# Kernel optimization log

Hardware: AMD Instinct MI355X
Metric: run time of the kernel (lower is better)

The kernel has to match this reference:

```python
import jax, jax.numpy as jnp
import numpy as np

G, NPG = 256, 128          # graphs per batch, nodes per graph
N = G * NPG                # 32768 total nodes
E = 524288                 # total directed edges; first half 'in', second half 'out'
DIN, D = 128, 256          # input feature dim, hidden dim
R = 200                    # num relations
C = 2                      # num classes
EPS = 1e-5                 # batchnorm eps


def setup_inputs() -> dict:
    key = jax.random.key(0)
    ks = jax.random.split(key, 20)

    def w(k, shape):
        fan_in = shape[-2] if len(shape) >= 2 else shape[-1]
        return jax.random.normal(k, shape, jnp.float32) / np.float32(np.sqrt(fan_in))

    return {
        "x": jax.random.normal(ks[0], (N, DIN), jnp.float32),
        "rel_emb": w(ks[1], (R, DIN)),
        # conv1: DIN -> D
        "w_in1": w(ks[2], (DIN, D)), "w_out1": w(ks[3], (DIN, D)),
        "w_loop1": w(ks[4], (DIN, D)), "w_rel1": w(ks[5], (DIN, D)),
        "loop_rel1": w(ks[6], (1, DIN)),
        "bias1": jnp.zeros((D,), jnp.float32),
        "gamma1": jnp.ones((D,), jnp.float32), "beta1": jnp.zeros((D,), jnp.float32),
        # conv2..conv5 stacked: D -> D
        "W_in": w(ks[7], (4, D, D)), "W_out": w(ks[8], (4, D, D)),
        "W_loop": w(ks[9], (4, D, D)), "W_rel": w(ks[10], (4, D, D)),
        "Loop_rel": w(ks[11], (4, 1, D)),
        "Bias": jnp.zeros((4, D), jnp.float32),
        "Gamma": jnp.ones((4, D), jnp.float32), "Beta": jnp.zeros((4, D), jnp.float32),
        # head: concat2 => Linear(4*D, C)
        "lin_w": w(ks[12], (4 * D, C)), "lin_b": jnp.zeros((C,), jnp.float32),
        # graph data (int constants)
        "edge_index": jax.random.randint(ks[13], (2, E), 0, N),
        "edge_type": jax.random.randint(ks[14], (E,), 0, R),
        "batch": jnp.repeat(jnp.arange(G, dtype=jnp.int32), NPG),
        "rel_labels": jax.random.randint(ks[15], (G,), 0, R),
    }


def _compgcn_conv(x, rel, edge_index, edge_type,
                  w_in, w_out, w_loop, w_rel, loop_rel, bias, gamma, beta):
    """One CompGCNConv layer (opn='mult', dropout=identity/eval, BN with batch stats)."""
    n = x.shape[0]
    half = edge_index.shape[1] // 2

    def direction(idx, etype, W):
        src, dst = idx[0], idx[1]
        # symmetric normalization: deg^{-1/2}[src] * deg^{-1/2}[dst]
        deg = jax.ops.segment_sum(jnp.ones_like(src, jnp.float32), src, num_segments=n)
        dinv = jnp.where(deg > 0, deg ** -0.5, 0.0)
        norm = dinv[src] * dinv[dst]                       # [half]
        msg = ((x[src] * rel[etype]) @ W) * norm[:, None]  # [half, D]
        return jax.ops.segment_sum(msg, dst, num_segments=n)

    in_res = direction(edge_index[:, :half], edge_type[:half], w_in)
    out_res = direction(edge_index[:, half:], edge_type[half:], w_out)
    loop_res = (x * loop_rel) @ w_loop                     # self-loop, loop relation, no norm

    out = (in_res + out_res + loop_res) / 3.0 + bias
    mean = out.mean(axis=0)
    var = out.var(axis=0)
    out = (out - mean) / jnp.sqrt(var + EPS) * gamma + beta
    return jax.nn.relu(out), rel @ w_rel


def reference(x, rel_emb, w_in1, w_out1, w_loop1, w_rel1, loop_rel1, bias1, gamma1, beta1,
              W_in, W_out, W_loop, W_rel, Loop_rel, Bias, Gamma, Beta,
              lin_w, lin_b, edge_index, edge_type, batch, rel_labels):
    x, r = _compgcn_conv(x, rel_emb, edge_index, edge_type,
                         w_in1, w_out1, w_loop1, w_rel1, loop_rel1, bias1, gamma1, beta1)
    for l in range(4):  # conv2..conv5 (fixed small layer loop)
        x, r = _compgcn_conv(x, r, edge_index, edge_type,
                             W_in[l], W_out[l], W_loop[l], W_rel[l],
                             Loop_rel[l], Bias[l], Gamma[l], Beta[l])

    # per-graph head/tail nodes (first two nodes of each graph) via segment offsets
    counts = jax.ops.segment_sum(jnp.ones((x.shape[0],), jnp.float32), batch, num_segments=G)
    offsets = (jnp.cumsum(counts) - counts).astype(jnp.int32)
    h_batch = x[offsets]
    t_batch = x[offsets + 1]

    pooled = jax.ops.segment_sum(x, batch, num_segments=G) / counts[:, None]
    rel_embs = r[rel_labels]

    feats = jnp.concatenate([pooled, rel_embs, h_batch, t_batch], axis=1)  # concat2 path
    return feats @ lin_w + lin_b


if __name__ == "__main__":
    out = reference(**setup_inputs())
    print(out.shape, out.dtype)
```

## Files before the change

kernel.cpp:

```cpp
#include <hip/hip_runtime.h>

#define NN 32768
#define GG 256
#define NPGN 128
#define ET 524288
#define EH 262144
#define D1 128
#define D2 256
#define RR 200

typedef unsigned short u16;
typedef __attribute__((ext_vector_type(8))) short bf16x8;
typedef __attribute__((ext_vector_type(4))) float f32x4;
typedef __attribute__((ext_vector_type(8))) unsigned short u16x8;

__device__ __forceinline__ float bf2f(u16 u) {
    union { unsigned int i; float f; } v; v.i = ((unsigned int)u) << 16; return v.f;
}
__device__ __forceinline__ u16 f2bf(float f) {
    union { unsigned int i; float f; } v; v.f = f;
    unsigned int x = v.i;
    return (u16)((x + 0x7fffu + ((x >> 16) & 1u)) >> 16);
}

__global__ void k_hist(const int* __restrict__ ei, int* __restrict__ hs_in,
                       int* __restrict__ hs_out, int* __restrict__ hd_in,
                       int* __restrict__ hd_out) {
    int e = blockIdx.x * blockDim.x + threadIdx.x;
    if (e >= ET) return;
    int s = ei[e], d = ei[ET + e];
    if (e < EH) { atomicAdd(&hs_in[s], 1);  atomicAdd(&hd_in[d], 1); }
    else        { atomicAdd(&hs_out[s], 1); atomicAdd(&hd_out[d], 1); }
}

__global__ void k_dinv(const int* __restrict__ hs_in, const int* __restrict__ hs_out,
                       float* __restrict__ dinv_in, float* __restrict__ dinv_out) {
    int n = blockIdx.x * blockDim.x + threadIdx.x;
    if (n >= NN) return;
    int a = hs_in[n], b = hs_out[n];
    dinv_in[n]  = a > 0 ? rsqrtf((float)a) : 0.f;
    dinv_out[n] = b > 0 ? rsqrtf((float)b) : 0.f;
}

__global__ __launch_bounds__(1024) void k_scan(const int* __restrict__ hist,
                                               int* __restrict__ off) {
    __shared__ int lds[1024];
    int t = threadIdx.x;
    int base = t * 32;
    int loc[32];
    int s = 0;
#pragma unroll
    for (int i = 0; i < 32; ++i) { loc[i] = s; s += hist[base + i]; }
    lds[t] = s;
    int tot = s;
    __syncthreads();
    for (int st = 1; st < 1024; st <<= 1) {
        int v = (t >= st) ? lds[t - st] : 0;
        __syncthreads();
        lds[t] += v;
        __syncthreads();
    }
    int excl = lds[t] - tot;
#pragma unroll
    for (int i = 0; i < 32; ++i) off[base + i] = excl + loc[i];
    if (t == 1023) off[NN] = lds[1023];
}

__global__ void k_fill(const int* __restrict__ ei, const int* __restrict__ et,
                       const float* __restrict__ dinv, const int* __restrict__ off,
                       int* __restrict__ cur, int* __restrict__ c_src,
                       int* __restrict__ c_et, float* __restrict__ c_norm, int eoff) {
    int e = blockIdx.x * blockDim.x + threadIdx.x;
    if (e >= EH) return;
    int s = ei[eoff + e], d = ei[ET + eoff + e], t = et[eoff + e];
    int slot = off[d] + atomicAdd(&cur[d], 1);
    c_src[slot] = s;
    c_et[slot] = t;
    c_norm[slot] = dinv[s] * dinv[d];
}

__global__ void k_convx(const float* __restrict__ in, u16* __restrict__ out, int n) {
    int i = blockIdx.x * blockDim.x + threadIdx.x;
    if (i < n) out[i] = f2bf(in[i]);
}

__global__ void k_prepw(const float* __restrict__ Wi, const float* __restrict__ Wo,
                        const float* __restrict__ Wl, const float* __restrict__ lr,
                        u16* __restrict__ WiT, u16* __restrict__ WoT,
                        u16* __restrict__ WlT, int K, int L) {
    int idx = blockIdx.x * blockDim.x + threadIdx.x;
    int per = L * K * 256;
    if (idx >= 3 * per) return;
    int fam = idx / per, rem = idx % per;
    int l = rem / (K * 256), rr = rem % (K * 256);
    int k = rr / 256, n = rr % 256;
    const float* src = fam == 0 ? Wi : fam == 1 ? Wo : Wl;
    float v = src[((size_t)l * K + k) * 256 + n];
    if (fam == 2) v *= lr[l * K + k];
    u16* dst = fam == 0 ? WiT : fam == 1 ? WoT : WlT;
    dst[((size_t)l * 256 + n) * K + k] = f2bf(v);
}

template <int K>
__global__ __launch_bounds__(256) void k_gather2(
    const u16* __restrict__ x, const u16* __restrict__ relb,
    const int* __restrict__ csI, const int* __restrict__ cetI,
    const float* __restrict__ cnI, const int* __restrict__ offI,
    const int* __restrict__ csO, const int* __restrict__ cetO,
    const float* __restrict__ cnO, const int* __restrict__ offO,
    u16* __restrict__ aggI, u16* __restrict__ aggO, float* __restrict__ bnsums) {
    if (blockIdx.x == 0 && blockIdx.y == 0 && threadIdx.x < 128)
        ((float4*)bnsums)[threadIdx.x] = make_float4(0.f, 0.f, 0.f, 0.f);
    constexpr int LPN = K / 8;
    constexpr int NPB = 256 / LPN;
    const int dir = blockIdx.y;
    const int* __restrict__ cs  = dir ? csO : csI;
    const int* __restrict__ cet = dir ? cetO : cetI;
    const float* __restrict__ cn = dir ? cnO : cnI;
    const int* __restrict__ off = dir ? offO : offI;
    u16* __restrict__ agg = dir ? aggO : aggI;

    int node = blockIdx.x * NPB + (threadIdx.x / LPN);
    int lane = threadIdx.x % LPN;
    int c = lane * 8;
    int e0 = off[node], e1 = off[node + 1];
    float acc[8] = {};
    int e = e0;
    for (; e + 4 <= e1; e += 4) {
        int s0 = cs[e],  s1 = cs[e + 1],  s2 = cs[e + 2],  s3 = cs[e + 3];
        int t0 = cet[e], t1 = cet[e + 1], t2 = cet[e + 2], t3 = cet[e + 3];
        float n0 = cn[e], n1 = cn[e + 1], n2 = cn[e + 2], n3 = cn[e + 3];
        u16x8 xa = *(const u16x8*)(x + (size_t)s0 * K + c);
        u16x8 xb = *(const u16x8*)(x + (size_t)s1 * K + c);
        u16x8 xc = *(const u16x8*)(x + (size_t)s2 * K + c);
        u16x8 xd = *(const u16x8*)(x + (size_t)s3 * K + c);
        u16x8 ra = *(const u16x8*)(relb + (size_t)t0 * K + c);
        u16x8 rb = *(const u16x8*)(relb + (size_t)t1 * K + c);
        u16x8 rc = *(const u16x8*)(relb + (size_t)t2 * K + c);
        u16x8 rd = *(const u16x8*)(relb + (size_t)t3 * K + c);
#pragma unroll
        for (int i = 0; i < 8; ++i)
            acc[i] += n0 * bf2f(xa[i]) * bf2f(ra[i]) + n1 * bf2f(xb[i]) * bf2f(rb[i])
                    + n2 * bf2f(xc[i]) * bf2f(rc[i]) + n3 * bf2f(xd[i]) * bf2f(rd[i]);
    }
    for (; e < e1; ++e) {
        int s0 = cs[e], t0 = cet[e]; float n0 = cn[e];
        u16x8 xa = *(const u16x8*)(x + (size_t)s0 * K + c);
        u16x8 ra = *(const u16x8*)(relb + (size_t)t0 * K + c);
#pragma unroll
        for (int i = 0; i < 8; ++i) acc[i] += n0 * bf2f(xa[i]) * bf2f(ra[i]);
    }
    u16x8 o;
#pragma unroll
    for (int i = 0; i < 8; ++i) o[i] = f2bf(acc[i]);
    *(u16x8*)(agg + (size_t)node * K + c) = o;
}

__device__ __forceinline__ void stage16(const u16* __restrict__ src, int baseRow,
                                        int K, int kk, u16* lds, int chunk, int lane) {
    int row = chunk * 16 + (lane >> 2);
    int ks  = (lane & 3) ^ ((lane >> 2) & 3);
    const u16* g = src + (size_t)(baseRow + row) * K + kk + ks * 8;
    __builtin_amdgcn_global_load_lds((const __attribute__((address_space(1))) void*)g,
                                     (__attribute__((address_space(3))) void*)(lds + chunk * 512),
                                     16, 0, 0);
}

template <int K>
__global__ __launch_bounds__(256) void k_gemm_mfma(
    const u16* __restrict__ A1, const u16* __restrict__ A2, const u16* __restrict__ A3,
    const u16* __restrict__ W1, const u16* __restrict__ W2, const u16* __restrict__ W3,
    const float* __restrict__ bias, u16* __restrict__ hb, float* __restrict__ bnsums) {
    __shared__ u16 As_s[2][128 * 32];
    __shared__ u16 Ws_s[2][128 * 32];
    const int tid = threadIdx.x;
    const int wave = tid >> 6, lane = tid & 63;
    const int q = lane >> 4, r = lane & 15;
    const int rowBlk = blockIdx.x * 128;
    const int colBlk = blockIdx.y * 128;
    const int rowBase = rowBlk + (wave & 1) * 64;
    const int colBase = colBlk + (wave >> 1) * 64;

    f32x4 zero = {0.f, 0.f, 0.f, 0.f};
    f32x4 acc[4][4];
#pragma unroll
    for (int i = 0; i < 4; ++i)
#pragma unroll
        for (int j = 0; j < 4; ++j) acc[i][j] = zero;

    const u16* As[3] = {A1, A2, A3};
    const u16* Ws[3] = {W1, W2, W3};
    constexpr int SPS = K / 32;
    constexpr int TOT = 3 * SPS;

    stage16(As[0], rowBlk, K, 0, As_s[0], 2 * wave, lane);
    stage16(As[0], rowBlk, K, 0, As_s[0], 2 * wave + 1, lane);
    stage16(Ws[0], colBlk, K, 0, Ws_s[0], 2 * wave, lane);
    stage16(Ws[0], colBlk, K, 0, Ws_s[0], 2 * wave + 1, lane);

    const int sw = (q ^ (r & 3)) * 8;
    for (int s = 0; s < TOT; ++s) {
        __syncthreads();
        if (s + 1 < TOT) {
            int seg = (s + 1) / SPS;
            int kk  = ((s + 1) % SPS) * 32;
            stage16(As[seg], rowBlk, K, kk, As_s[(s + 1) & 1], 2 * wave, lane);
            stage16(As[seg], rowBlk, K, kk, As_s[(s + 1) & 1], 2 * wave + 1, lane);
            stage16(Ws[seg], colBlk, K, kk, Ws_s[(s + 1) & 1], 2 * wave, lane);
            stage16(Ws[seg], colBlk, K, kk, Ws_s[(s + 1) & 1], 2 * wave + 1, lane);
        }
        const u16* al = As_s[s & 1] + (wave & 1) * 64 * 32;
        const u16* wl = Ws_s[s & 1] + (wave >> 1) * 64 * 32;
        bf16x8 a[4], b[4];
#pragma unroll
        for (int t = 0; t < 4; ++t) {
            a[t] = *(const bf16x8*)(al + (t * 16 + r) * 32 + sw);
            b[t] = *(const bf16x8*)(wl + (t * 16 + r) * 32 + sw);
        }
#pragma unroll
        for (int tm = 0; tm < 4; ++tm)
#pragma unroll
            for (int tn = 0; tn < 4; ++tn)
                acc[tm][tn] = __builtin_amdgcn_mfma_f32_16x16x32_bf16(
                    a[tm], b[tn], acc[tm][tn], 0, 0, 0);
    }

#pragma unroll
    for (int tn = 0; tn < 4; ++tn) {
        int col = colBase + tn * 16 + r;
        float bv = bias[col];
        float sv = 0.f, qv = 0.f;
#pragma unroll
        for (int tm = 0; tm < 4; ++tm) {
#pragma unroll
            for (int reg = 0; reg < 4; ++reg) {
                int row = rowBase + tm * 16 + q * 4 + reg;
                float v = acc[tm][tn][reg] * (1.0f / 3.0f) + bv;
                hb[(size_t)row * 256 + col] = f2bf(v);
                sv += v; qv += v * v;
            }
        }
        sv += __shfl_xor(sv, 16); sv += __shfl_xor(sv, 32);
        qv += __shfl_xor(qv, 16); qv += __shfl_xor(qv, 32);
        if (q == 0) {
            atomicAdd(&bnsums[col], sv);
            atomicAdd(&bnsums[256 + col], qv);
        }
    }
}

__global__ __launch_bounds__(256) void k_gemm_rel(
    const float* __restrict__ A, const float* __restrict__ W,
    float* __restrict__ C, u16* __restrict__ Cb, int M, int K) {
    __shared__ float As[16][68];
    __shared__ float Wshm[16][68];
    const int tid = threadIdx.x;
    const int tx = tid & 15, ty = tid >> 4;
    const int arow = tid >> 2;
    const int akc  = (tid & 3) << 2;
    const int wk   = tid >> 4;
    const int wn0  = (tid & 15) << 2;
    const int rowBase = blockIdx.x << 6;
    const int colBase = blockIdx.y << 6;
    float acc[4][4] = {};
    for (int k0 = 0; k0 < K; k0 += 16) {
        float4 av = make_float4(0.f, 0.f, 0.f, 0.f);
        int rr = rowBase + arow;
        if (rr < M) av = *(const float4*)(A + (size_t)rr * K + k0 + akc);
        As[akc + 0][arow] = av.x;
        As[akc + 1][arow] = av.y;
        As[akc + 2][arow] = av.z;
        As[akc + 3][arow] = av.w;
        float4 wv = *(const float4*)(W + (size_t)(k0 + wk) * D2 + colBase + wn0);
        Wshm[wk][wn0 + 0] = wv.x;
        Wshm[wk][wn0 + 1] = wv.y;
        Wshm[wk][wn0 + 2] = wv.z;
        Wshm[wk][wn0 + 3] = wv.w;
        __syncthreads();
#pragma unroll
        for (int kk = 0; kk < 16; ++kk) {
            float a0 = As[kk][(ty << 2) + 0], a1 = As[kk][(ty << 2) + 1];
            float a2 = As[kk][(ty << 2) + 2], a3 = As[kk][(ty << 2) + 3];
            float w0 = Wshm[kk][(tx << 2) + 0], w1 = Wshm[kk][(tx << 2) + 1];
            float w2 = Wshm[kk][(tx << 2) + 2], w3 = Wshm[kk][(tx << 2) + 3];
            acc[0][0] += a0 * w0; acc[0][1] += a0 * w1; acc[0][2] += a0 * w2; acc[0][3] += a0 * w3;
            acc[1][0] += a1 * w0; acc[1][1] += a1 * w1; acc[1][2] += a1 * w2; acc[1][3] += a1 * w3;
            acc[2][0] += a2 * w0; acc[2][1] += a2 * w1; acc[2][2] += a2 * w2; acc[2][3] += a2 * w3;
            acc[3][0] += a3 * w0; acc[3][1] += a3 * w1; acc[3][2] += a3 * w2; acc[3][3] += a3 * w3;
        }
        __syncthreads();
    }
#pragma unroll
    for (int i = 0; i < 4; ++i) {
        int rr = rowBase + (ty << 2) + i;
        if (rr >= M) continue;
        float* cp = C + (size_t)rr * D2 + colBase + (tx << 2);
        u16* cb = Cb + (size_t)rr * D2 + colBase + (tx << 2);
        cp[0] = acc[i][0]; cp[1] = acc[i][1]; cp[2] = acc[i][2]; cp[3] = acc[i][3];
        cb[0] = f2bf(acc[i][0]); cb[1] = f2bf(acc[i][1]);
        cb[2] = f2bf(acc[i][2]); cb[3] = f2bf(acc[i][3]);
    }
}

__global__ void k_bnapply(const u16x8* __restrict__ hb8, const float* __restrict__ sums,
                          const float* __restrict__ gamma, const float* __restrict__ beta,
                          u16x8* __restrict__ xb8) {
    int idx = blockIdx.x * blockDim.x + threadIdx.x;
    int f0 = (idx & 31) << 3;
    u16x8 v = hb8[idx];
    u16x8 o;
#pragma unroll
    for (int i = 0; i < 8; ++i) {
        int f = f0 + i;
        float mean = sums[f] * (1.0f / NN);
        float var  = sums[256 + f] * (1.0f / NN) - mean * mean;
        float inv  = 1.0f / sqrtf(var + 1e-5f);
        float t = (bf2f(v[i]) - mean) * inv * gamma[f] + beta[f];
        o[i] = f2bf(t > 0.f ? t : 0.f);
    }
    xb8[idx] = o;
}

__global__ void k_feats(const u16* __restrict__ x, const float* __restrict__ rel,
                        const int* __restrict__ rel_labels, float* __restrict__ feats) {
    int g = blockIdx.x, f = threadIdx.x;
    const u16* xg = x + (size_t)g * NPGN * D2;
    float s = 0.f;
#pragma unroll 8
    for (int n = 0; n < NPGN; ++n) s += bf2f(xg[(size_t)n * D2 + f]);
    float* fg = feats + (size_t)g * 1024;
    fg[f]       = s * (1.0f / NPGN);
    fg[256 + f] = rel[(size_t)rel_labels[g] * D2 + f];
    fg[512 + f] = bf2f(xg[f]);
    fg[768 + f] = bf2f(xg[D2 + f]);
}

__global__ void k_head(const float* __restrict__ feats, const float* __restrict__ lw,
                       const float* __restrict__ lb, float* __restrict__ out) {
    int g = blockIdx.x, t = threadIdx.x;
    __shared__ float s0[256], s1[256];
    float a0 = 0.f, a1 = 0.f;
#pragma unroll
    for (int j = 0; j < 4; ++j) {
        int k = t * 4 + j;
        float fv = feats[(size_t)g * 1024 + k];
        a0 += fv * lw[k * 2 + 0];
        a1 += fv * lw[k * 2 + 1];
    }
    s0[t] = a0; s1[t] = a1;
    __syncthreads();
    for (int s = 128; s > 0; s >>= 1) {
        if (t < s) { s0[t] += s0[t + s]; s1[t] += s1[t + s]; }
        __syncthreads();
    }
    if (t == 0) {
        out[g * 2 + 0] = s0[0] + lb[0];
        out[g * 2 + 1] = s1[0] + lb[1];
    }
}

extern "C" void kernel_launch(void* const* d_in, const int* in_sizes, int n_in,
                              void* d_out, int out_size, void* d_ws, size_t ws_size,
                              hipStream_t stream) {
    const float* x0   = (const float*)d_in[0];
    const float* rel0 = (const float*)d_in[1];
    const int* edge_index = (const int*)d_in[20];
    const int* edge_type  = (const int*)d_in[21];
    const int* rel_labels = (const int*)d_in[23];
    float* out = (float*)d_out;

    float* ws = (float*)d_ws;
    float* relA  = ws;
    float* relB  = relA + (size_t)RR * 256;
    float* dinv_in  = relB + (size_t)RR * 256;
    float* dinv_out = dinv_in + NN;
    float* cnorm_in  = dinv_out + NN;
    float* cnorm_out = cnorm_in + EH;
    float* bnsums    = cnorm_out + EH;
    float* feats     = bnsums + 512;
    int* csrc_in  = (int*)(feats + GG * 1024);
    int* cet_in   = csrc_in + EH;
    int* csrc_out = cet_in + EH;
    int* cet_out  = csrc_out + EH;
    int* off_in   = cet_out + EH;
    int* off_out  = off_in + NN + 8;
    int* hs_in    = off_out + NN + 8;
    int* hs_out   = hs_in + NN;
    int* hd_in    = hs_out + NN;
    int* hd_out   = hd_in + NN;
    int* cur_in   = hd_out + NN;
    int* cur_out  = cur_in + NN;
    u16* xbf0 = (u16*)(cur_out + NN);
    u16* xbfA = xbf0 + (size_t)NN * 128;
    u16* aggI = xbfA + (size_t)NN * 256;
    u16* aggO = aggI + (size_t)NN * 256;
    u16* hb   = aggO + (size_t)NN * 256;
    u16* wt0  = hb + (size_t)NN * 256;
    u16* wtS  = wt0 + 3 * 256 * 128;
    u16* relbf = wtS + 12 * 65536;

    hipMemsetAsync(hs_in, 0, 6 * NN * sizeof(int), stream);
    k_hist<<<ET / 256, 256, 0, stream>>>(edge_index, hs_in, hs_out, hd_in, hd_out);
    k_dinv<<<NN / 256, 256, 0, stream>>>(hs_in, hs_out, dinv_in, dinv_out);
    k_scan<<<1, 1024, 0, stream>>>(hd_in, off_in);
    k_scan<<<1, 1024, 0, stream>>>(hd_out, off_out);
    k_fill<<<EH / 256, 256, 0, stream>>>(edge_index, edge_type, dinv_in, off_in,
                                         cur_in, csrc_in, cet_in, cnorm_in, 0);
    k_fill<<<EH / 256, 256, 0, stream>>>(edge_index, edge_type, dinv_out, off_out,
                                         cur_out, csrc_out, cet_out, cnorm_out, EH);
    k_convx<<<(NN * D1) / 256, 256, 0, stream>>>(x0, xbf0, NN * D1);
    k_convx<<<(RR * D1 + 255) / 256, 256, 0, stream>>>(rel0, relbf, RR * D1);
    k_prepw<<<(3 * D1 * 256) / 256, 256, 0, stream>>>(
        (const float*)d_in[2], (const float*)d_in[3], (const float*)d_in[4],
        (const float*)d_in[6], wt0, wt0 + 256 * D1, wt0 + 2 * 256 * D1, D1, 1);
    k_prepw<<<(3 * 4 * D2 * 256) / 256, 256, 0, stream>>>(
        (const float*)d_in[10], (const float*)d_in[11], (const float*)d_in[12],
        (const float*)d_in[14], wtS, wtS + 4 * 65536, wtS + 8 * 65536, D2, 4);

    const float* rc = rel0; float* rn = relA;

    for (int l = 0; l < 5; ++l) {
        const int K = (l == 0) ? D1 : D2;
        const u16* xb = (l == 0) ? xbf0 : xbfA;
        const u16 *WiT, *WoT, *WlT;
        const float *Wr, *bias, *gamma, *beta;
        if (l == 0) {
            WiT = wt0; WoT = wt0 + 256 * D1; WlT = wt0 + 2 * 256 * D1;
            Wr = (const float*)d_in[5];
            bias  = (const float*)d_in[7];
            gamma = (const float*)d_in[8];
            beta  = (const float*)d_in[9];
        } else {
            int m = l - 1;
            WiT = wtS + (size_t)m * 65536;
            WoT = wtS + (size_t)(4 + m) * 65536;
            WlT = wtS + (size_t)(8 + m) * 65536;
            Wr = (const float*)d_in[13] + (size_t)m * D2 * D2;
            bias  = (const float*)d_in[15] + (size_t)m * D2;
            gamma = (const float*)d_in[16] + (size_t)m * D2;
            beta  = (const float*)d_in[17] + (size_t)m * D2;
        }

        if (K == D1) {
            dim3 ggr(NN / 16, 2);
            k_gather2<D1><<<ggr, 256, 0, stream>>>(xb, relbf, csrc_in, cet_in,
                cnorm_in, off_in, csrc_out, cet_out, cnorm_out, off_out, aggI, aggO, bnsums);
        } else {
            dim3 ggr(NN / 8, 2);
            k_gather2<D2><<<ggr, 256, 0, stream>>>(xb, relbf, csrc_in, cet_in,
                cnorm_in, off_in, csrc_out, cet_out, cnorm_out, off_out, aggI, aggO, bnsums);
        }
        dim3 ggrid(NN / 128, 2);
        if (K == D1) k_gemm_mfma<D1><<<ggrid, 256, 0, stream>>>(aggI, aggO, xb, WiT, WoT, WlT, bias, hb, bnsums);
        else         k_gemm_mfma<D2><<<ggrid, 256, 0, stream>>>(aggI, aggO, xb, WiT, WoT, WlT, bias, hb, bnsums);
        k_bnapply<<<(NN * 256 / 8) / 256, 256, 0, stream>>>((const u16x8*)hb, bnsums,
                                                            gamma, beta, (u16x8*)xbfA);
        k_gemm_rel<<<dim3(4, 4), 256, 0, stream>>>(rc, Wr, rn, relbf, RR, K);
        const float* nr = rn;
        rn = (l == 0) ? relB : (float*)rc;
        rc = nr;
    }

    k_feats<<<GG, 256, 0, stream>>>(xbfA, rc, rel_labels, feats);
    k_head<<<GG, 256, 0, stream>>>(feats, (const float*)d_in[18],
                                   (const float*)d_in[19], out);
}
```

Baseline: 812.2 us.

## Double-buffer gather edge loads and shrink GEMM column tile to 64

The gather kernel now loads the next group of four edges into a second register set while it computes on the current group. The tail loop is gone: out-of-range edges are clamped to the last valid index and given zero weight. This is meant to hide gather latency. Separately, the MFMA GEMM tile goes from 128x128 to 128x64 and the grid is doubled in y, which gives more blocks for occupancy but re-reads A tiles twice as often and doubles the BN atomics.

```diff
diff --git a/kernel.cpp b/kernel.cpp
--- a/kernel.cpp
+++ b/kernel.cpp
@@ -125,30 +125,44 @@
     int c = lane * 8;
     int e0 = off[node], e1 = off[node + 1];
     float acc[8] = {};
-    int e = e0;
-    for (; e + 4 <= e1; e += 4) {
-        int s0 = cs[e],  s1 = cs[e + 1],  s2 = cs[e + 2],  s3 = cs[e + 3];
-        int t0 = cet[e], t1 = cet[e + 1], t2 = cet[e + 2], t3 = cet[e + 3];
-        float n0 = cn[e], n1 = cn[e + 1], n2 = cn[e + 2], n3 = cn[e + 3];
-        u16x8 xa = *(const u16x8*)(x + (size_t)s0 * K + c);
-        u16x8 xb = *(const u16x8*)(x + (size_t)s1 * K + c);
-        u16x8 xc = *(const u16x8*)(x + (size_t)s2 * K + c);
-        u16x8 xd = *(const u16x8*)(x + (size_t)s3 * K + c);
-        u16x8 ra = *(const u16x8*)(relb + (size_t)t0 * K + c);
-        u16x8 rb = *(const u16x8*)(relb + (size_t)t1 * K + c);
-        u16x8 rc = *(const u16x8*)(relb + (size_t)t2 * K + c);
-        u16x8 rd = *(const u16x8*)(relb + (size_t)t3 * K + c);
+
+    u16x8 xA[4], rA[4], xB[4], rB[4];
+    float nA[4], nB[4];
+
+    auto loadg = [&](u16x8* xv, u16x8* rv, float* nv, int g) {
+#pragma unroll
+        for (int j = 0; j < 4; ++j) {
+            int ee = (g + j < e1) ? (g + j) : (e1 - 1);
+            nv[j] = (g + j < e1) ? cn[ee] : 0.f;
+            int s = cs[ee], t = cet[ee];
+            xv[j] = *(const u16x8*)(x + (size_t)s * K + c);
+            rv[j] = *(const u16x8*)(relb + (size_t)t * K + c);
+        }
+    };
+    auto compg = [&](u16x8* xv, u16x8* rv, float* nv) {
 #pragma unroll
         for (int i = 0; i < 8; ++i)
-            acc[i] += n0 * bf2f(xa[i]) * bf2f(ra[i]) + n1 * bf2f(xb[i]) * bf2f(rb[i])
-                    + n2 * bf2f(xc[i]) * bf2f(rc[i]) + n3 * bf2f(xd[i]) * bf2f(rd[i]);
-    }
-    for (; e < e1; ++e) {
-        int s0 = cs[e], t0 = cet[e]; float n0 = cn[e];
-        u16x8 xa = *(const u16x8*)(x + (size_t)s0 * K + c);
-        u16x8 ra = *(const u16x8*)(relb + (size_t)t0 * K + c);
-#pragma unroll
-        for (int i = 0; i < 8; ++i) acc[i] += n0 * bf2f(xa[i]) * bf2f(ra[i]);
+            acc[i] += nv[0] * bf2f(xv[0][i]) * bf2f(rv[0][i])
+                    + nv[1] * bf2f(xv[1][i]) * bf2f(rv[1][i])
+                    + nv[2] * bf2f(xv[2][i]) * bf2f(rv[2][i])
+                    + nv[3] * bf2f(xv[3][i]) * bf2f(rv[3][i]);
+    };
+
+    if (e0 < e1) {
+        loadg(xA, rA, nA, e0);
+        int g = e0;
+        while (true) {
+            int gn = g + 4;
+            if (gn < e1) loadg(xB, rB, nB, gn);
+            compg(xA, rA, nA);
+            g = gn;
+            if (g >= e1) break;
+            gn = g + 4;
+            if (gn < e1) loadg(xA, rA, nA, gn);
+            compg(xB, rB, nB);
+            g = gn;
+            if (g >= e1) break;
+        }
     }
     u16x8 o;
 #pragma unroll
@@ -172,21 +186,21 @@
     const u16* __restrict__ W1, const u16* __restrict__ W2, const u16* __restrict__ W3,
     const float* __restrict__ bias, u16* __restrict__ hb, float* __restrict__ bnsums) {
     __shared__ u16 As_s[2][128 * 32];
-    __shared__ u16 Ws_s[2][128 * 32];
+    __shared__ u16 Ws_s[2][64 * 32];
     const int tid = threadIdx.x;
     const int wave = tid >> 6, lane = tid & 63;
     const int q = lane >> 4, r = lane & 15;
     const int rowBlk = blockIdx.x * 128;
-    const int colBlk = blockIdx.y * 128;
+    const int colBlk = blockIdx.y * 64;
     const int rowBase = rowBlk + (wave & 1) * 64;
-    const int colBase = colBlk + (wave >> 1) * 64;
+    const int colSub  = (wave >> 1) * 32;
 
     f32x4 zero = {0.f, 0.f, 0.f, 0.f};
-    f32x4 acc[4][4];
+    f32x4 acc[4][2];
 #pragma unroll
     for (int i = 0; i < 4; ++i)
 #pragma unroll
-        for (int j = 0; j < 4; ++j) acc[i][j] = zero;
+        for (int j = 0; j < 2; ++j) acc[i][j] = zero;
 
     const u16* As[3] = {A1, A2, A3};
     const u16* Ws[3] = {W1, W2, W3};
@@ -195,8 +209,7 @@
 
     stage16(As[0], rowBlk, K, 0, As_s[0], 2 * wave, lane);
     stage16(As[0], rowBlk, K, 0, As_s[0], 2 * wave + 1, lane);
-    stage16(Ws[0], colBlk, K, 0, Ws_s[0], 2 * wave, lane);
-    stage16(Ws[0], colBlk, K, 0, Ws_s[0], 2 * wave + 1, lane);
+    stage16(Ws[0], colBlk, K, 0, Ws_s[0], wave, lane);
 
     const int sw = (q ^ (r & 3)) * 8;
     for (int s = 0; s < TOT; ++s) {
@@ -206,28 +219,26 @@
             int kk  = ((s + 1) % SPS) * 32;
             stage16(As[seg], rowBlk, K, kk, As_s[(s + 1) & 1], 2 * wave, lane);
             stage16(As[seg], rowBlk, K, kk, As_s[(s + 1) & 1], 2 * wave + 1, lane);
-            stage16(Ws[seg], colBlk, K, kk, Ws_s[(s + 1) & 1], 2 * wave, lane);
-            stage16(Ws[seg], colBlk, K, kk, Ws_s[(s + 1) & 1], 2 * wave + 1, lane);
+            stage16(Ws[seg], colBlk, K, kk, Ws_s[(s + 1) & 1], wave, lane);
         }
         const u16* al = As_s[s & 1] + (wave & 1) * 64 * 32;
-        const u16* wl = Ws_s[s & 1] + (wave >> 1) * 64 * 32;
-        bf16x8 a[4], b[4];
-#pragma unroll
-        for (int t = 0; t < 4; ++t) {
-            a[t] = *(const bf16x8*)(al + (t * 16 + r) * 32 + sw);
-            b[t] = *(const bf16x8*)(wl + (t * 16 + r) * 32 + sw);
-        }
+        const u16* wl = Ws_s[s & 1] + colSub * 32;
+        bf16x8 a[4], b[2];
+#pragma unroll
+        for (int t = 0; t < 4; ++t) a[t] = *(const bf16x8*)(al + (t * 16 + r) * 32 + sw);
+#pragma unroll
+        for (int t = 0; t < 2; ++t) b[t] = *(const bf16x8*)(wl + (t * 16 + r) * 32 + sw);
 #pragma unroll
         for (int tm = 0; tm < 4; ++tm)
 #pragma unroll
-            for (int tn = 0; tn < 4; ++tn)
+            for (int tn = 0; tn < 2; ++tn)
                 acc[tm][tn] = __builtin_amdgcn_mfma_f32_16x16x32_bf16(
                     a[tm], b[tn], acc[tm][tn], 0, 0, 0);
     }
 
 #pragma unroll
-    for (int tn = 0; tn < 4; ++tn) {
-        int col = colBase + tn * 16 + r;
+    for (int tn = 0; tn < 2; ++tn) {
+        int col = colBlk + colSub + tn * 16 + r;
         float bv = bias[col];
         float sv = 0.f, qv = 0.f;
 #pragma unroll
@@ -450,7 +461,7 @@
             k_gather2<D2><<<ggr, 256, 0, stream>>>(xb, relbf, csrc_in, cet_in,
                 cnorm_in, off_in, csrc_out, cet_out, cnorm_out, off_out, aggI, aggO, bnsums);
         }
-        dim3 ggrid(NN / 128, 2);
+        dim3 ggrid(NN / 128, 4);
         if (K == D1) k_gemm_mfma<D1><<<ggrid, 256, 0, stream>>>(aggI, aggO, xb, WiT, WoT, WlT, bias, hb, bnsums);
         else         k_gemm_mfma<D2><<<ggrid, 256, 0, stream>>>(aggI, aggO, xb, WiT, WoT, WlT, bias, hb, bnsums);
         k_bnapply<<<(NN * 256 / 8) / 256, 256, 0, stream>>>((const u16x8*)hb, bnsums,
```

Result: slower. 892.4 us (+9.9%).

## Split gather by 64-column chunks and narrow GEMM column tile to 64

Applied to the files above, without the earlier changes.

The gather kernel now gives each node 8 lanes covering a 64-column slice and uses a third grid dimension over column chunks. This gives the same per-thread shape for both layer widths and spreads each node's edge loop over more blocks. The MFMA GEMM tile shrinks from 128x128 to 128x64, doubling block count and halving accumulator registers, which raises occupancy and parallelism. The cost is that edge indices and A tiles are re-read once per column chunk, adding redundant global traffic.

```diff
diff --git a/kernel.cpp b/kernel.cpp
--- a/kernel.cpp
+++ b/kernel.cpp
@@ -109,10 +109,8 @@
     const int* __restrict__ csO, const int* __restrict__ cetO,
     const float* __restrict__ cnO, const int* __restrict__ offO,
     u16* __restrict__ aggI, u16* __restrict__ aggO, float* __restrict__ bnsums) {
-    if (blockIdx.x == 0 && blockIdx.y == 0 && threadIdx.x < 128)
+    if (blockIdx.x == 0 && blockIdx.y == 0 && blockIdx.z == 0 && threadIdx.x < 128)
         ((float4*)bnsums)[threadIdx.x] = make_float4(0.f, 0.f, 0.f, 0.f);
-    constexpr int LPN = K / 8;
-    constexpr int NPB = 256 / LPN;
     const int dir = blockIdx.y;
     const int* __restrict__ cs  = dir ? csO : csI;
     const int* __restrict__ cet = dir ? cetO : cetI;
@@ -120,9 +118,8 @@
     const int* __restrict__ off = dir ? offO : offI;
     u16* __restrict__ agg = dir ? aggO : aggI;
 
-    int node = blockIdx.x * NPB + (threadIdx.x / LPN);
-    int lane = threadIdx.x % LPN;
-    int c = lane * 8;
+    int node = blockIdx.x * 32 + (threadIdx.x >> 3);
+    int c = blockIdx.z * 64 + (threadIdx.x & 7) * 8;
     int e0 = off[node], e1 = off[node + 1];
     float acc[8] = {};
     int e = e0;
@@ -172,21 +169,21 @@
     const u16* __restrict__ W1, const u16* __restrict__ W2, const u16* __restrict__ W3,
     const float* __restrict__ bias, u16* __restrict__ hb, float* __restrict__ bnsums) {
     __shared__ u16 As_s[2][128 * 32];
-    __shared__ u16 Ws_s[2][128 * 32];
+    __shared__ u16 Ws_s[2][64 * 32];
     const int tid = threadIdx.x;
     const int wave = tid >> 6, lane = tid & 63;
     const int q = lane >> 4, r = lane & 15;
     const int rowBlk = blockIdx.x * 128;
-    const int colBlk = blockIdx.y * 128;
+    const int colBlk = blockIdx.y * 64;
     const int rowBase = rowBlk + (wave & 1) * 64;
-    const int colBase = colBlk + (wave >> 1) * 64;
+    const int colSub  = (wave >> 1) * 32;
 
     f32x4 zero = {0.f, 0.f, 0.f, 0.f};
-    f32x4 acc[4][4];
+    f32x4 acc[4][2];
 #pragma unroll
     for (int i = 0; i < 4; ++i)
 #pragma unroll
-        for (int j = 0; j < 4; ++j) acc[i][j] = zero;
+        for (int j = 0; j < 2; ++j) acc[i][j] = zero;
 
     const u16* As[3] = {A1, A2, A3};
     const u16* Ws[3] = {W1, W2, W3};
@@ -195,8 +192,7 @@
 
     stage16(As[0], rowBlk, K, 0, As_s[0], 2 * wave, lane);
     stage16(As[0], rowBlk, K, 0, As_s[0], 2 * wave + 1, lane);
-    stage16(Ws[0], colBlk, K, 0, Ws_s[0], 2 * wave, lane);
-    stage16(Ws[0], colBlk, K, 0, Ws_s[0], 2 * wave + 1, lane);
+    stage16(Ws[0], colBlk, K, 0, Ws_s[0], wave, lane);
 
     const int sw = (q ^ (r & 3)) * 8;
     for (int s = 0; s < TOT; ++s) {
@@ -206,28 +202,26 @@
             int kk  = ((s + 1) % SPS) * 32;
             stage16(As[seg], rowBlk, K, kk, As_s[(s + 1) & 1], 2 * wave, lane);
             stage16(As[seg], rowBlk, K, kk, As_s[(s + 1) & 1], 2 * wave + 1, lane);
-            stage16(Ws[seg], colBlk, K, kk, Ws_s[(s + 1) & 1], 2 * wave, lane);
-            stage16(Ws[seg], colBlk, K, kk, Ws_s[(s + 1) & 1], 2 * wave + 1, lane);
+            stage16(Ws[seg], colBlk, K, kk, Ws_s[(s + 1) & 1], wave, lane);
         }
         const u16* al = As_s[s & 1] + (wave & 1) * 64 * 32;
-        const u16* wl = Ws_s[s & 1] + (wave >> 1) * 64 * 32;
-        bf16x8 a[4], b[4];
-#pragma unroll
-        for (int t = 0; t < 4; ++t) {
-            a[t] = *(const bf16x8*)(al + (t * 16 + r) * 32 + sw);
-            b[t] = *(const bf16x8*)(wl + (t * 16 + r) * 32 + sw);
-        }
+        const u16* wl = Ws_s[s & 1] + colSub * 32;
+        bf16x8 a[4], b[2];
+#pragma unroll
+        for (int t = 0; t < 4; ++t) a[t] = *(const bf16x8*)(al + (t * 16 + r) * 32 + sw);
+#pragma unroll
+        for (int t = 0; t < 2; ++t) b[t] = *(const bf16x8*)(wl + (t * 16 + r) * 32 + sw);
 #pragma unroll
         for (int tm = 0; tm < 4; ++tm)
 #pragma unroll
-            for (int tn = 0; tn < 4; ++tn)
+            for (int tn = 0; tn < 2; ++tn)
                 acc[tm][tn] = __builtin_amdgcn_mfma_f32_16x16x32_bf16(
                     a[tm], b[tn], acc[tm][tn], 0, 0, 0);
     }
 
 #pragma unroll
-    for (int tn = 0; tn < 4; ++tn) {
-        int col = colBase + tn * 16 + r;
+    for (int tn = 0; tn < 2; ++tn) {
+        int col = colBlk + colSub + tn * 16 + r;
         float bv = bias[col];
         float sv = 0.f, qv = 0.f;
 #pragma unroll
@@ -441,16 +435,12 @@
             beta  = (const float*)d_in[17] + (size_t)m * D2;
         }
 
-        if (K == D1) {
-            dim3 ggr(NN / 16, 2);
-            k_gather2<D1><<<ggr, 256, 0, stream>>>(xb, relbf, csrc_in, cet_in,
-                cnorm_in, off_in, csrc_out, cet_out, cnorm_out, off_out, aggI, aggO, bnsums);
-        } else {
-            dim3 ggr(NN / 8, 2);
-            k_gather2<D2><<<ggr, 256, 0, stream>>>(xb, relbf, csrc_in, cet_in,
-                cnorm_in, off_in, csrc_out, cet_out, cnorm_out, off_out, aggI, aggO, bnsums);
-        }
-        dim3 ggrid(NN / 128, 2);
+        dim3 ggr(NN / 32, 2, K / 64);
+        if (K == D1) k_gather2<D1><<<ggr, 256, 0, stream>>>(xb, relbf, csrc_in, cet_in,
+            cnorm_in, off_in, csrc_out, cet_out, cnorm_out, off_out, aggI, aggO, bnsums);
+        else         k_gather2<D2><<<ggr, 256, 0, stream>>>(xb, relbf, csrc_in, cet_in,
+            cnorm_in, off_in, csrc_out, cet_out, cnorm_out, off_out, aggI, aggO, bnsums);
+        dim3 ggrid(NN / 128, 4);
         if (K == D1) k_gemm_mfma<D1><<<ggrid, 256, 0, stream>>>(aggI, aggO, xb, WiT, WoT, WlT, bias, hb, bnsums);
         else         k_gemm_mfma<D2><<<ggrid, 256, 0, stream>>>(aggI, aggO, xb, WiT, WoT, WlT, bias, hb, bnsums);
         k_bnapply<<<(NN * 256 / 8) / 256, 256, 0, stream>>>((const u16x8*)hb, bnsums,
```

Result: slower. 901.8 us (+11.0%).
